# Optimization experiments

Hardware: AMD Instinct MI355X
Metric: run time of the kernel (lower is better)

## Reference

```python
import jax, jax.numpy as jnp
import numpy as np

N_NODES = 50000
N_EDGES = 800000
HIDDEN = 64
DEPTH = 3
NUM_GRAPHS = 256
NUM_CLASSES = 1
BN_EPS = 1e-5


def setup_inputs() -> dict:
    key = jax.random.key(0)
    ks = jax.random.split(key, 12)
    x = jax.random.normal(ks[0], (N_NODES, HIDDEN), dtype=jnp.float32)
    edge_index = jax.random.randint(ks[1], (2, N_EDGES), 0, N_NODES, dtype=jnp.int32)
    batch = jnp.sort(jax.random.randint(ks[2], (N_NODES,), 0, NUM_GRAPHS, dtype=jnp.int32))
    s = 1.0 / np.sqrt(HIDDEN)
    W1 = jax.random.uniform(ks[3], (DEPTH, HIDDEN, HIDDEN), jnp.float32, -s, s)
    b1 = jax.random.uniform(ks[4], (DEPTH, HIDDEN), jnp.float32, -s, s)
    W2 = jax.random.uniform(ks[5], (DEPTH, HIDDEN, HIDDEN), jnp.float32, -s, s)
    b2 = jax.random.uniform(ks[6], (DEPTH, HIDDEN), jnp.float32, -s, s)
    gamma = jnp.ones((DEPTH, HIDDEN), jnp.float32)
    beta = jnp.zeros((DEPTH, HIDDEN), jnp.float32)
    Wf = jax.random.uniform(ks[7], (HIDDEN, NUM_CLASSES), jnp.float32, -s, s)
    bf = jax.random.uniform(ks[8], (NUM_CLASSES,), jnp.float32, -s, s)
    return {"x": x, "edge_index": edge_index, "batch": batch,
            "W1": W1, "b1": b1, "W2": W2, "b2": b2,
            "gamma": gamma, "beta": beta, "Wf": Wf, "bf": bf}


def reference(x, edge_index, batch, W1, b1, W2, b2, gamma, beta, Wf, bf):
    src, dst = edge_index[0], edge_index[1]
    for i in range(DEPTH):
        # GINConv: (1+eps)*x + scatter-add of neighbor features (eps=0)
        agg = jnp.zeros_like(x).at[dst].add(x[src])
        h = x + agg
        h = jax.nn.relu(h @ W1[i] + b1[i])
        h = jax.nn.relu(h @ W2[i] + b2[i])
        # BatchNorm over node dimension (training-mode batch stats)
        mean = h.mean(axis=0)
        var = ((h - mean) ** 2).mean(axis=0)
        h = (h - mean) * jax.lax.rsqrt(var + BN_EPS) * gamma[i] + beta[i]
        x = jax.nn.relu(h)
    pooled = jax.ops.segment_sum(x, batch, num_segments=NUM_GRAPHS)  # [G, H]
    return pooled @ Wf + bf
```

## Files before the change

### kernel.cpp

```cpp
#include <hip/hip_runtime.h>

#define HIDDEN_C 64
#define NCHUNK 256

typedef __attribute__((ext_vector_type(8))) short bf16x8;
typedef __attribute__((ext_vector_type(8))) unsigned short u16x8;
typedef __attribute__((ext_vector_type(4))) float f32x4;

__device__ __forceinline__ float4 f4zero() { return make_float4(0.f, 0.f, 0.f, 0.f); }

__device__ __forceinline__ unsigned short f2bf(float f) {
    unsigned u = __float_as_uint(f);
    u += 0x7FFF + ((u >> 16) & 1);
    return (unsigned short)(u >> 16);
}
__device__ __forceinline__ float bf2f(unsigned short h) {
    return __uint_as_float(((unsigned)h) << 16);
}
__device__ __forceinline__ unsigned short f2h(float f) {
    _Float16 h = (_Float16)f;
    unsigned short u;
    __builtin_memcpy(&u, &h, 2);
    return u;
}
__device__ __forceinline__ float h2f(unsigned short u) {
    _Float16 h;
    __builtin_memcpy(&h, &u, 2);
    return (float)h;
}

__device__ __forceinline__ int swz_idx(int row, int k) {
    return row * 64 + ((((k >> 3) ^ (row & 7)) << 3) | (k & 7));
}

__global__ __launch_bounds__(256) void k_xcvt(const float4* __restrict__ in,
                                              ushort4* __restrict__ out, int n4) {
    int i = blockIdx.x * 256 + threadIdx.x;
    if (i < n4) {
        float4 v = in[i];
        ushort4 o;
        o.x = f2h(v.x); o.y = f2h(v.y); o.z = f2h(v.z); o.w = f2h(v.w);
        out[i] = o;
    }
}

__global__ __launch_bounds__(256) void k_blocksum(const int* __restrict__ deg,
                                                  int* __restrict__ partial, int n) {
    int base = blockIdx.x * 1024 + threadIdx.x * 4;
    int s = 0;
#pragma unroll
    for (int k = 0; k < 4; ++k) {
        int i = base + k;
        if (i < n) s += deg[i];
    }
    __shared__ int red[256];
    red[threadIdx.x] = s;
    __syncthreads();
    for (int d = 128; d > 0; d >>= 1) {
        if (threadIdx.x < d) red[threadIdx.x] += red[threadIdx.x + d];
        __syncthreads();
    }
    if (threadIdx.x == 0) partial[blockIdx.x] = red[0];
}

__global__ __launch_bounds__(256) void k_scanpartial(int* __restrict__ partial,
                                                     int* __restrict__ last_slot,
                                                     int nBlocks, int nE) {
    __shared__ int buf[256];
    int tid = threadIdx.x;
    int v = (tid < nBlocks) ? partial[tid] : 0;
    buf[tid] = v;
    __syncthreads();
    for (int d = 1; d < 256; d <<= 1) {
        int t = (tid >= d) ? buf[tid - d] : 0;
        __syncthreads();
        buf[tid] += t;
        __syncthreads();
    }
    if (tid < nBlocks) partial[tid] = buf[tid] - v;
    if (tid == 0) last_slot[0] = nE;
}

__global__ __launch_bounds__(256) void k_writeptr(const int* __restrict__ deg,
                                                  const int* __restrict__ partial,
                                                  int* __restrict__ outp, int n) {
    int tid = threadIdx.x;
    int base = blockIdx.x * 1024 + tid * 4;
    int d[4];
    int s = 0;
#pragma unroll
    for (int k = 0; k < 4; ++k) {
        int i = base + k;
        d[k] = (i < n) ? deg[i] : 0;
        s += d[k];
    }
    __shared__ int buf[256];
    buf[tid] = s;
    __syncthreads();
    for (int dd = 1; dd < 256; dd <<= 1) {
        int t = (tid >= dd) ? buf[tid - dd] : 0;
        __syncthreads();
        buf[tid] += t;
        __syncthreads();
    }
    int off = partial[blockIdx.x] + buf[tid] - s;
#pragma unroll
    for (int k = 0; k < 4; ++k) {
        int i = base + k;
        if (i < n) {
            outp[i] = off;
            off += d[k];
        }
    }
}

__global__ __launch_bounds__(256) void k_bcount(const int* __restrict__ dst,
                                                int* __restrict__ cnt,
                                                int nE, int chunkSz, int nBuckets) {
    __shared__ int h[1024];
    int c = blockIdx.x, tid = threadIdx.x;
    for (int i = tid; i < nBuckets; i += 256) h[i] = 0;
    __syncthreads();
    int beg = c * chunkSz;
    int end = beg + chunkSz; if (end > nE) end = nE;
    int e = beg + tid;
    for (; e + 256 < end; e += 512) {
        int d0 = dst[e];
        int d1 = dst[e + 256];
        atomicAdd(&h[d0 >> 6], 1);
        atomicAdd(&h[d1 >> 6], 1);
    }
    if (e < end) atomicAdd(&h[dst[e] >> 6], 1);
    __syncthreads();
    for (int i = tid; i < nBuckets; i += 256) cnt[i * NCHUNK + c] = h[i];
}

__global__ __launch_bounds__(256) void k_bscatter(const int* __restrict__ src,
                                                  const int* __restrict__ dst,
                                                  const int* __restrict__ eoff,
                                                  unsigned* __restrict__ ebuf,
                                                  int nE, int chunkSz, int nBuckets) {
    __shared__ int cur[1024];
    int c = blockIdx.x, tid = threadIdx.x;
    for (int i = tid; i < nBuckets; i += 256) cur[i] = eoff[i * NCHUNK + c];
    __syncthreads();
    int beg = c * chunkSz;
    int end = beg + chunkSz; if (end > nE) end = nE;
    int e = beg + tid;
    for (; e + 256 < end; e += 512) {
        int d0 = dst[e];
        int d1 = dst[e + 256];
        int s0 = src[e];
        int s1 = src[e + 256];
        int p0 = atomicAdd(&cur[d0 >> 6], 1);
        int p1 = atomicAdd(&cur[d1 >> 6], 1);
        ebuf[p0] = ((unsigned)(d0 & 63) << 16) | (unsigned)s0;
        ebuf[p1] = ((unsigned)(d1 & 63) << 16) | (unsigned)s1;
    }
    if (e < end) {
        int d = dst[e];
        int pos = atomicAdd(&cur[d >> 6], 1);
        ebuf[pos] = ((unsigned)(d & 63) << 16) | (unsigned)src[e];
    }
}

__global__ __launch_bounds__(256) void k_bfill(const unsigned* __restrict__ ebuf,
                                               const int* __restrict__ eoff,
                                               int* __restrict__ rowptr,
                                               int* __restrict__ col,
                                               int nNodes, int nE, int nBuckets) {
    __shared__ int deg[64], cur[64];
    int b = blockIdx.x, tid = threadIdx.x;
    int lo = eoff[b * NCHUNK];
    int hi = (b + 1 < nBuckets) ? eoff[(b + 1) * NCHUNK] : nE;
    if (tid < 64) deg[tid] = 0;
    __syncthreads();
    for (int e = lo + tid; e < hi; e += 256) atomicAdd(&deg[ebuf[e] >> 16], 1);
    __syncthreads();
    if (tid < 64) {
        int d = deg[tid];
        int s = d;
        for (int o = 1; o < 64; o <<= 1) {
            int t = __shfl_up(s, o, 64);
            if (tid >= o) s += t;
        }
        int st = s - d;
        cur[tid] = lo + st;
        int node = b * 64 + tid;
        if (node < nNodes) rowptr[node] = lo + st;
    }
    __syncthreads();
    for (int e = lo + tid; e < hi; e += 256) {
        unsigned pk = ebuf[e];
        int pos = atomicAdd(&cur[pk >> 16], 1);
        col[pos] = (int)(pk & 0xFFFFu);
    }
}

__global__ __launch_bounds__(256) void k_wprep(const float* __restrict__ W1,
                                               const float* __restrict__ W2,
                                               unsigned short* __restrict__ wt) {
    __shared__ unsigned short s[8192];
    int b = blockIdx.x;
    int layer = b >> 1;
    const float* src = ((b & 1) ? W2 : W1) + (size_t)layer * 4096;
    int tid = threadIdx.x;
    int k = tid >> 2;
    int f0 = (tid & 3) * 16;
    const float* srcp = src + k * 64 + f0;
#pragma unroll
    for (int j4 = 0; j4 < 4; ++j4) {
        float4 wv = *(const float4*)(srcp + j4 * 4);
        float c[4] = {wv.x, wv.y, wv.z, wv.w};
        int f = f0 + j4 * 4;
#pragma unroll
        for (int j = 0; j < 4; ++j) {
            unsigned short h = f2bf(c[j]);
            int ix = swz_idx(f + j, k);
            s[ix] = h;
            s[4096 + ix] = f2bf(c[j] - bf2f(h));
        }
    }
    __syncthreads();
    uint4* dst = (uint4*)(wt + (size_t)b * 8192);
    const uint4* sp = (const uint4*)s;
#pragma unroll
    for (int it = 0; it < 4; ++it) dst[it * 256 + tid] = sp[it * 256 + tid];
}

__global__ __launch_bounds__(256) void k_statred(const float* __restrict__ pstat,
                                                 float* __restrict__ stats, int nb) {
    int j = blockIdx.x;
    int tid = threadIdx.x;
    float s = 0.f;
    for (int b = tid; b < nb; b += 256) s += pstat[(size_t)b * 128 + j];
    __shared__ float red[256];
    red[tid] = s;
    __syncthreads();
    for (int d = 128; d > 0; d >>= 1) {
        if (tid < d) red[tid] += red[tid + d];
        __syncthreads();
    }
    if (tid == 0) stats[j] = red[0];
}

template <bool DOBN>
__global__ __launch_bounds__(256) void k_aggbn(const unsigned short* __restrict__ x16,
                                               const int* __restrict__ rowptr,
                                               const int* __restrict__ col,
                                               const float* __restrict__ stats,
                                               const float* __restrict__ gamma,
                                               const float* __restrict__ beta,
                                               unsigned short* __restrict__ hout,
                                               int nNodes, float invN) {
    int wid = threadIdx.x >> 6;
    int lane = threadIdx.x & 63;
    int g8 = lane >> 3;
    int l8 = lane & 7;
    int n = blockIdx.x * 4 + wid;
    if (n >= nNodes) return;

    float sc[8], sh[8];
    if (DOBN) {
#pragma unroll
        for (int j = 0; j < 8; ++j) {
            int f = l8 * 8 + j;
            float m = stats[f] * invN;
            float var = stats[64 + f] * invN - m * m;
            sc[j] = gamma[f] * rsqrtf(var + 1e-5f);
            sh[j] = beta[f] - m * sc[j];
        }
    }

#define LOADROW8(IDX, OP)                                                    \
    {                                                                        \
        u16x8 uv = *(const u16x8*)(x16 + (size_t)(IDX) * 64 + l8 * 8);       \
        _Pragma("unroll")                                                    \
        for (int j = 0; j < 8; ++j) {                                        \
            float v = h2f(uv[j]);                                            \
            if (DOBN) v = fmaxf(fmaf(v, sc[j], sh[j]), 0.f);                 \
            OP;                                                              \
        }                                                                    \
    }

    float acc[8] = {0.f, 0.f, 0.f, 0.f, 0.f, 0.f, 0.f, 0.f};
    if (g8 == 0) {
        LOADROW8(n, acc[j] = v)
    }

    int lo = rowptr[n], hi = rowptr[n + 1];
    int e = lo;
    for (; e + 16 <= hi; e += 16) {
        int i0 = col[e + g8];
        int i1 = col[e + 8 + g8];
        float t[8];
        LOADROW8(i0, t[j] = v)
        LOADROW8(i1, t[j] += v)
#pragma unroll
        for (int j = 0; j < 8; ++j) acc[j] += t[j];
    }
    for (; e + 8 <= hi; e += 8) {
        int i0 = col[e + g8];
        LOADROW8(i0, acc[j] += v)
    }
    if (e < hi) {
        int ee = e + g8;
        bool ok = ee < hi;
        int idx = col[ok ? ee : (hi - 1)];
        float t[8];
        LOADROW8(idx, t[j] = v)
        if (ok) {
#pragma unroll
            for (int j = 0; j < 8; ++j) acc[j] += t[j];
        }
    }
#undef LOADROW8

#pragma unroll
    for (int j = 0; j < 8; ++j) {
        acc[j] += __shfl_xor(acc[j], 8, 64);
        acc[j] += __shfl_xor(acc[j], 16, 64);
        acc[j] += __shfl_xor(acc[j], 32, 64);
    }

    if (lane < 8) {
        u16x8 o;
#pragma unroll
        for (int j = 0; j < 8; ++j) o[j] = f2h(acc[j]);
        *(u16x8*)(hout + (size_t)n * 64 + lane * 8) = o;
    }
}

__global__ __launch_bounds__(256, 5) void k_mlp(const unsigned short* __restrict__ h_in,
                                                unsigned short* __restrict__ h_out,
                                                const unsigned short* __restrict__ wt1,
                                                const float* __restrict__ b1,
                                                const unsigned short* __restrict__ wt2,
                                                const float* __restrict__ b2,
                                                float* __restrict__ pstat,
                                                int nNodes) {
    __shared__ __align__(16) unsigned short smem16[16384];
    unsigned short* sA_hi = smem16;
    unsigned short* sA_lo = smem16 + 4096;
    unsigned short* sW_hi = smem16 + 8192;
    unsigned short* sW_lo = smem16 + 12288;

    int tid = threadIdx.x;
    int n0 = blockIdx.x * 64;
    int lane = tid & 63;
    int w = tid >> 6;
    int lr = lane & 15;
    int q = lane >> 4;
    int r0 = w * 16;

    uint4 w2r[4];
#pragma unroll
    for (int it = 0; it < 4; ++it) w2r[it] = ((const uint4*)wt2)[it * 256 + tid];

#pragma unroll
    for (int it = 0; it < 2; ++it) {
        int idx = it * 256 + tid;
        int row = idx >> 3, ch = idx & 7;
        u16x8 iv = (u16x8)(0);
        if (n0 + row < nNodes)
            iv = *(const u16x8*)(h_in + (size_t)(n0 + row) * 64 + ch * 8);
        u16x8 hv, lv;
#pragma unroll
        for (int j = 0; j < 8; ++j) {
            float f = h2f(iv[j]);
            unsigned short h = f2bf(f);
            hv[j] = h;
            lv[j] = f2bf(f - bf2f(h));
        }
        int off = row * 64 + ((ch ^ (row & 7)) << 3);
        *(u16x8*)(sA_hi + off) = hv;
        *(u16x8*)(sA_lo + off) = lv;
    }
    {
        uint4* d = (uint4*)sW_hi;
        const uint4* s = (const uint4*)wt1;
#pragma unroll
        for (int it = 0; it < 4; ++it) d[it * 256 + tid] = s[it * 256 + tid];
    }
    __syncthreads();

    f32x4 acc[4];

#define GEMM_SPLIT(BIAS)                                                         \
    {                                                                            \
        int rowA = r0 + lr;                                                      \
        const unsigned short* pah = sA_hi + rowA * 64;                           \
        const unsigned short* pal = sA_lo + rowA * 64;                           \
        int sr = rowA & 7;                                                       \
        bf16x8 ah0 = *(const bf16x8*)(pah + ((q ^ sr) << 3));                    \
        bf16x8 ah1 = *(const bf16x8*)(pah + (((4 + q) ^ sr) << 3));              \
        bf16x8 al0 = *(const bf16x8*)(pal + ((q ^ sr) << 3));                    \
        bf16x8 al1 = *(const bf16x8*)(pal + (((4 + q) ^ sr) << 3));              \
        _Pragma("unroll")                                                        \
        for (int ct = 0; ct < 4; ++ct) {                                         \
            int f = ct * 16 + lr;                                                \
            const unsigned short* pbh = sW_hi + f * 64;                          \
            const unsigned short* pbl = sW_lo + f * 64;                          \
            int sf = f & 7;                                                      \
            bf16x8 bh0 = *(const bf16x8*)(pbh + ((q ^ sf) << 3));                \
            bf16x8 bh1 = *(const bf16x8*)(pbh + (((4 + q) ^ sf) << 3));          \
            bf16x8 bl0 = *(const bf16x8*)(pbl + ((q ^ sf) << 3));                \
            bf16x8 bl1 = *(const bf16x8*)(pbl + (((4 + q) ^ sf) << 3));          \
            float bias = BIAS[f];                                                \
            f32x4 c = {bias, bias, bias, bias};                                  \
            c = __builtin_amdgcn_mfma_f32_16x16x32_bf16(al0, bh0, c, 0, 0, 0);   \
            c = __builtin_amdgcn_mfma_f32_16x16x32_bf16(al1, bh1, c, 0, 0, 0);   \
            c = __builtin_amdgcn_mfma_f32_16x16x32_bf16(ah0, bl0, c, 0, 0, 0);   \
            c = __builtin_amdgcn_mfma_f32_16x16x32_bf16(ah1, bl1, c, 0, 0, 0);   \
            c = __builtin_amdgcn_mfma_f32_16x16x32_bf16(ah0, bh0, c, 0, 0, 0);   \
            c = __builtin_amdgcn_mfma_f32_16x16x32_bf16(ah1, bh1, c, 0, 0, 0);   \
            acc[ct] = c;                                                         \
        }                                                                        \
    }

    GEMM_SPLIT(b1)

    __syncthreads();

#pragma unroll
    for (int ct = 0; ct < 4; ++ct) {
        int f = ct * 16 + lr;
#pragma unroll
        for (int rg = 0; rg < 4; ++rg) {
            int row = r0 + q * 4 + rg;
            float v = fmaxf(acc[ct][rg], 0.f);
            unsigned short h = f2bf(v);
            int ix = swz_idx(row, f);
            sA_hi[ix] = h;
            sA_lo[ix] = f2bf(v - bf2f(h));
        }
    }
    {
        uint4* d = (uint4*)sW_hi;
#pragma unroll
        for (int it = 0; it < 4; ++it) d[it * 256 + tid] = w2r[it];
    }
    __syncthreads();

    GEMM_SPLIT(b2)

    __syncthreads();
#undef GEMM_SPLIT

    float* sS = (float*)sW_hi;
    float* sQ = sS + 256;

#pragma unroll
    for (int ct = 0; ct < 4; ++ct) {
        int f = ct * 16 + lr;
        float sp = 0.f, qp = 0.f;
#pragma unroll
        for (int rg = 0; rg < 4; ++rg) {
            int row = r0 + q * 4 + rg;
            float v = fmaxf(acc[ct][rg], 0.f);
            if (n0 + row < nNodes) {
                unsigned short hv = f2h(v);
                h_out[(size_t)(n0 + row) * 64 + f] = hv;
                float vq = h2f(hv);
                sp += vq;
                qp += vq * vq;
            }
        }
        sp += __shfl_xor(sp, 16, 64); qp += __shfl_xor(qp, 16, 64);
        sp += __shfl_xor(sp, 32, 64); qp += __shfl_xor(qp, 32, 64);
        if (q == 0) {
            sS[w * 64 + f] = sp;
            sQ[w * 64 + f] = qp;
        }
    }
    __syncthreads();
    if (tid < 128) {
        float v;
        if (tid < 64)
            v = sS[tid] + sS[64 + tid] + sS[128 + tid] + sS[192 + tid];
        else {
            int f = tid - 64;
            v = sQ[f] + sQ[64 + f] + sQ[128 + f] + sQ[192 + f];
        }
        pstat[(size_t)blockIdx.x * 128 + tid] = v;
    }
}

__device__ __forceinline__ int lower_bound_dev(const int* a, int n, int key) {
    int lo = 0, hi = n;
    while (lo < hi) {
        int mid = (lo + hi) >> 1;
        if (a[mid] < key) lo = mid + 1; else hi = mid;
    }
    return lo;
}

__global__ __launch_bounds__(256) void k_pool(const unsigned short* __restrict__ x16,
                                              const int* __restrict__ batch,
                                              const float* __restrict__ stats,
                                              const float* __restrict__ gamma,
                                              const float* __restrict__ beta,
                                              const float* __restrict__ Wf,
                                              const float* __restrict__ bf,
                                              float* __restrict__ out,
                                              int nNodes, float invN) {
    int wid = threadIdx.x >> 6;
    int lane = threadIdx.x & 63;
    int grp = lane >> 4;
    int l16 = lane & 15;
    int g = blockIdx.x * 4 + wid;

    float4 sc, sh;
    {
        float4 s  = ((const float4*)stats)[l16];
        float4 q  = ((const float4*)stats)[16 + l16];
        float4 ga = ((const float4*)gamma)[l16];
        float4 be = ((const float4*)beta)[l16];
        float m;
        m = s.x * invN; sc.x = ga.x * rsqrtf(q.x * invN - m * m + 1e-5f); sh.x = be.x - m * sc.x;
        m = s.y * invN; sc.y = ga.y * rsqrtf(q.y * invN - m * m + 1e-5f); sh.y = be.y - m * sc.y;
        m = s.z * invN; sc.z = ga.z * rsqrtf(q.z * invN - m * m + 1e-5f); sh.z = be.z - m * sc.z;
        m = s.w * invN; sc.w = ga.w * rsqrtf(q.w * invN - m * m + 1e-5f); sh.w = be.w - m * sc.w;
    }

    int lo = lower_bound_dev(batch, nNodes, g);
    int hi = lower_bound_dev(batch, nNodes, g + 1);

    float4 acc = f4zero();
    for (int r = lo + grp; r < hi; r += 4) {
        ushort4 uv = *(const ushort4*)(x16 + (size_t)r * 64 + l16 * 4);
        acc.x += fmaxf(fmaf(h2f(uv.x), sc.x, sh.x), 0.f);
        acc.y += fmaxf(fmaf(h2f(uv.y), sc.y, sh.y), 0.f);
        acc.z += fmaxf(fmaf(h2f(uv.z), sc.z, sh.z), 0.f);
        acc.w += fmaxf(fmaf(h2f(uv.w), sc.w, sh.w), 0.f);
    }
    acc.x += __shfl_xor(acc.x, 16, 64); acc.y += __shfl_xor(acc.y, 16, 64);
    acc.z += __shfl_xor(acc.z, 16, 64); acc.w += __shfl_xor(acc.w, 16, 64);
    acc.x += __shfl_xor(acc.x, 32, 64); acc.y += __shfl_xor(acc.y, 32, 64);
    acc.z += __shfl_xor(acc.z, 32, 64); acc.w += __shfl_xor(acc.w, 32, 64);

    float4 wf = ((const float4*)Wf)[l16];
    float p = acc.x * wf.x + acc.y * wf.y + acc.z * wf.z + acc.w * wf.w;
    p += __shfl_xor(p, 1, 64);
    p += __shfl_xor(p, 2, 64);
    p += __shfl_xor(p, 4, 64);
    p += __shfl_xor(p, 8, 64);
    if (lane == 0) out[g] = p + bf[0];
}

extern "C" void kernel_launch(void* const* d_in, const int* in_sizes, int n_in,
                              void* d_out, int out_size, void* d_ws, size_t ws_size,
                              hipStream_t stream) {
    const float* x_in  = (const float*)d_in[0];
    const int*   ei    = (const int*)d_in[1];
    const int*   batch = (const int*)d_in[2];
    const float* W1    = (const float*)d_in[3];
    const float* b1    = (const float*)d_in[4];
    const float* W2    = (const float*)d_in[5];
    const float* b2    = (const float*)d_in[6];
    const float* gamma = (const float*)d_in[7];
    const float* beta  = (const float*)d_in[8];
    const float* Wf    = (const float*)d_in[9];
    const float* bf    = (const float*)d_in[10];

    const int nNodes = in_sizes[0] / HIDDEN_C;
    const int nE = in_sizes[1] / 2;
    const int* src = ei;
    const int* dst = ei + nE;

    const int nBuckets = (nNodes + 63) / 64;
    const int nTot = nBuckets * NCHUNK;
    const int chunkSz = (nE + NCHUNK - 1) / NCHUNK;
    const int scanBlocks = (nTot + 1023) / 1024;
    const float invN = 1.f / (float)nNodes;

    const size_t NH = ((size_t)nNodes * HIDDEN_C * sizeof(unsigned short) + 255) & ~(size_t)255;
    char* ws = (char*)d_ws;
    unsigned short* x16 = (unsigned short*)ws;
    unsigned short* hA  = (unsigned short*)(ws + NH);
    unsigned short* hB  = (unsigned short*)(ws + 2 * NH);
    float*    stats   = (float*)(ws + 3 * NH);
    unsigned short* wtbuf = (unsigned short*)(ws + 3 * NH + 4096);
    float*    pstat   = (float*)(ws + 3 * NH + 4096 + 98304);
    int*      rowptr  = (int*)((char*)pstat + 409600);
    int*      partial = rowptr + nNodes + 64;
    int*      col     = partial + 256;
    unsigned* ebuf    = (unsigned*)hB;
    int*      cnt     = (int*)((char*)hB + (size_t)nE * 4);
    int*      eoff    = cnt + nTot + 64;

    const int mlpGrid = nBuckets;
    const int aggGrid = (nNodes + 3) / 4;
    const int cvtGrid = (nNodes * 16 + 255) / 256;

    k_xcvt<<<cvtGrid, 256, 0, stream>>>((const float4*)x_in, (ushort4*)x16, nNodes * 16);
    k_wprep<<<6, 256, 0, stream>>>(W1, W2, wtbuf);
    k_bcount<<<NCHUNK, 256, 0, stream>>>(dst, cnt, nE, chunkSz, nBuckets);
    k_blocksum<<<scanBlocks, 256, 0, stream>>>(cnt, partial, nTot);
    k_scanpartial<<<1, 256, 0, stream>>>(partial, rowptr + nNodes, scanBlocks, nE);
    k_writeptr<<<scanBlocks, 256, 0, stream>>>(cnt, partial, eoff, nTot);
    k_bscatter<<<NCHUNK, 256, 0, stream>>>(src, dst, eoff, ebuf, nE, chunkSz, nBuckets);
    k_bfill<<<nBuckets, 256, 0, stream>>>(ebuf, eoff, rowptr, col, nNodes, nE, nBuckets);

    const unsigned short* prev_h = x16;
    unsigned short* cur = hA;
    for (int i = 0; i < 3; ++i) {
        if (i == 0) {
            k_aggbn<false><<<aggGrid, 256, 0, stream>>>(prev_h, rowptr, col,
                                                        nullptr, nullptr, nullptr,
                                                        cur, nNodes, invN);
        } else {
            k_aggbn<true><<<aggGrid, 256, 0, stream>>>(prev_h, rowptr, col,
                                                       stats + (size_t)(i - 1) * 128,
                                                       gamma + (size_t)(i - 1) * 64,
                                                       beta + (size_t)(i - 1) * 64,
                                                       cur, nNodes, invN);
        }
        k_mlp<<<mlpGrid, 256, 0, stream>>>(cur, cur,
                                           wtbuf + (size_t)(2 * i) * 8192, b1 + (size_t)i * 64,
                                           wtbuf + (size_t)(2 * i + 1) * 8192, b2 + (size_t)i * 64,
                                           pstat, nNodes);
        k_statred<<<128, 256, 0, stream>>>(pstat, stats + (size_t)i * 128, nBuckets);
        prev_h = cur;
        cur = (cur == hA) ? hB : hA;
    }

    k_pool<<<64, 256, 0, stream>>>(prev_h, batch, stats + 256, gamma + 128, beta + 128,
                                   Wf, bf, (float*)d_out, nNodes, invN);
}
```

Before: 196.4 us.

## Fuse CSR-build preprocessing kernels and replace per-chunk offsets with global atomic bucket cursors

```diff
diff --git a/kernel.cpp b/kernel.cpp
--- a/kernel.cpp
+++ b/kernel.cpp
@@ -33,90 +33,105 @@
     return row * 64 + ((((k >> 3) ^ (row & 7)) << 3) | (k & 7));
 }
 
-__global__ __launch_bounds__(256) void k_xcvt(const float4* __restrict__ in,
-                                              ushort4* __restrict__ out, int n4) {
-    int i = blockIdx.x * 256 + threadIdx.x;
+__global__ __launch_bounds__(256) void k_prep(const float4* __restrict__ xin4,
+                                              ushort4* __restrict__ x16o, int n4,
+                                              const float* __restrict__ W1,
+                                              const float* __restrict__ W2,
+                                              unsigned short* __restrict__ wt,
+                                              const int* __restrict__ dst,
+                                              int* __restrict__ gTot,
+                                              int nE, int chunkSz, int nBuckets) {
+    __shared__ unsigned short s[8192];
+    __shared__ int h[1024];
+    int b = blockIdx.x, tid = threadIdx.x;
+
+    int i = b * 256 + tid;
     if (i < n4) {
-        float4 v = in[i];
+        float4 v = xin4[i];
         ushort4 o;
         o.x = f2h(v.x); o.y = f2h(v.y); o.z = f2h(v.z); o.w = f2h(v.w);
-        out[i] = o;
-    }
-}
-
-__global__ __launch_bounds__(256) void k_blocksum(const int* __restrict__ deg,
-                                                  int* __restrict__ partial, int n) {
-    int base = blockIdx.x * 1024 + threadIdx.x * 4;
-    int s = 0;
-#pragma unroll
-    for (int k = 0; k < 4; ++k) {
-        int i = base + k;
-        if (i < n) s += deg[i];
-    }
-    __shared__ int red[256];
-    red[threadIdx.x] = s;
-    __syncthreads();
-    for (int d = 128; d > 0; d >>= 1) {
-        if (threadIdx.x < d) red[threadIdx.x] += red[threadIdx.x + d];
+        x16o[i] = o;
+    }
+
+    if (b < 6) {
+        int layer = b >> 1;
+        const float* src = ((b & 1) ? W2 : W1) + (size_t)layer * 4096;
+        int k = tid >> 2;
+        int f0 = (tid & 3) * 16;
+        const float* srcp = src + k * 64 + f0;
+#pragma unroll
+        for (int j4 = 0; j4 < 4; ++j4) {
+            float4 wv = *(const float4*)(srcp + j4 * 4);
+            float c[4] = {wv.x, wv.y, wv.z, wv.w};
+            int f = f0 + j4 * 4;
+#pragma unroll
+            for (int j = 0; j < 4; ++j) {
+                unsigned short hh = f2bf(c[j]);
+                int ix = swz_idx(f + j, k);
+                s[ix] = hh;
+                s[4096 + ix] = f2bf(c[j] - bf2f(hh));
+            }
+        }
         __syncthreads();
-    }
-    if (threadIdx.x == 0) partial[blockIdx.x] = red[0];
-}
-
-__global__ __launch_bounds__(256) void k_scanpartial(int* __restrict__ partial,
-                                                     int* __restrict__ last_slot,
-                                                     int nBlocks, int nE) {
-    __shared__ int buf[256];
+        uint4* dstw = (uint4*)(wt + (size_t)b * 8192);
+        const uint4* sp = (const uint4*)s;
+#pragma unroll
+        for (int it = 0; it < 4; ++it) dstw[it * 256 + tid] = sp[it * 256 + tid];
+    }
+
+    if (b < NCHUNK) {
+        for (int j = tid; j < nBuckets; j += 256) h[j] = 0;
+        __syncthreads();
+        int beg = b * chunkSz;
+        int end = beg + chunkSz; if (end > nE) end = nE;
+        int e = beg + tid;
+        for (; e + 256 < end; e += 512) {
+            int d0 = dst[e];
+            int d1 = dst[e + 256];
+            atomicAdd(&h[d0 >> 6], 1);
+            atomicAdd(&h[d1 >> 6], 1);
+        }
+        if (e < end) atomicAdd(&h[dst[e] >> 6], 1);
+        __syncthreads();
+        for (int j = tid; j < nBuckets; j += 256) {
+            int c = h[j];
+            if (c) atomicAdd(&gTot[j], c);
+        }
+    }
+}
+
+__global__ __launch_bounds__(1024) void k_bscan(const int* __restrict__ gTot,
+                                                int* __restrict__ gBase,
+                                                int* __restrict__ gCur,
+                                                int* __restrict__ rowptr,
+                                                int nBuckets, int nNodes, int nE) {
+    __shared__ int buf[1024];
     int tid = threadIdx.x;
-    int v = (tid < nBlocks) ? partial[tid] : 0;
+    int v = (tid < nBuckets) ? gTot[tid] : 0;
     buf[tid] = v;
     __syncthreads();
-    for (int d = 1; d < 256; d <<= 1) {
+    for (int d = 1; d < 1024; d <<= 1) {
         int t = (tid >= d) ? buf[tid - d] : 0;
         __syncthreads();
         buf[tid] += t;
         __syncthreads();
     }
-    if (tid < nBlocks) partial[tid] = buf[tid] - v;
-    if (tid == 0) last_slot[0] = nE;
-}
-
-__global__ __launch_bounds__(256) void k_writeptr(const int* __restrict__ deg,
-                                                  const int* __restrict__ partial,
-                                                  int* __restrict__ outp, int n) {
-    int tid = threadIdx.x;
-    int base = blockIdx.x * 1024 + tid * 4;
-    int d[4];
-    int s = 0;
-#pragma unroll
-    for (int k = 0; k < 4; ++k) {
-        int i = base + k;
-        d[k] = (i < n) ? deg[i] : 0;
-        s += d[k];
-    }
-    __shared__ int buf[256];
-    buf[tid] = s;
-    __syncthreads();
-    for (int dd = 1; dd < 256; dd <<= 1) {
-        int t = (tid >= dd) ? buf[tid - dd] : 0;
-        __syncthreads();
-        buf[tid] += t;
-        __syncthreads();
-    }
-    int off = partial[blockIdx.x] + buf[tid] - s;
-#pragma unroll
-    for (int k = 0; k < 4; ++k) {
-        int i = base + k;
-        if (i < n) {
-            outp[i] = off;
-            off += d[k];
-        }
-    }
-}
-
-__global__ __launch_bounds__(256) void k_bcount(const int* __restrict__ dst,
-                                                int* __restrict__ cnt,
-                                                int nE, int chunkSz, int nBuckets) {
+    if (tid < nBuckets) {
+        int ex = buf[tid] - v;
+        gBase[tid] = ex;
+        gCur[tid] = ex;
+    }
+    if (tid == 0) {
+        gBase[nBuckets] = nE;
+        rowptr[nNodes] = nE;
+    }
+}
+
+__global__ __launch_bounds__(256) void k_bscatter(const int* __restrict__ src,
+                                                  const int* __restrict__ dst,
+                                                  int* __restrict__ gCur,
+                                                  unsigned* __restrict__ ebuf,
+                                                  int nE, int chunkSz, int nBuckets) {
     __shared__ int h[1024];
     int c = blockIdx.x, tid = threadIdx.x;
     for (int i = tid; i < nBuckets; i += 256) h[i] = 0;
@@ -125,54 +140,43 @@
     int end = beg + chunkSz; if (end > nE) end = nE;
     int e = beg + tid;
     for (; e + 256 < end; e += 512) {
-        int d0 = dst[e];
-        int d1 = dst[e + 256];
-        atomicAdd(&h[d0 >> 6], 1);
-        atomicAdd(&h[d1 >> 6], 1);
+        atomicAdd(&h[dst[e] >> 6], 1);
+        atomicAdd(&h[dst[e + 256] >> 6], 1);
     }
     if (e < end) atomicAdd(&h[dst[e] >> 6], 1);
     __syncthreads();
-    for (int i = tid; i < nBuckets; i += 256) cnt[i * NCHUNK + c] = h[i];
-}
-
-__global__ __launch_bounds__(256) void k_bscatter(const int* __restrict__ src,
-                                                  const int* __restrict__ dst,
-                                                  const int* __restrict__ eoff,
-                                                  unsigned* __restrict__ ebuf,
-                                                  int nE, int chunkSz, int nBuckets) {
-    __shared__ int cur[1024];
-    int c = blockIdx.x, tid = threadIdx.x;
-    for (int i = tid; i < nBuckets; i += 256) cur[i] = eoff[i * NCHUNK + c];
-    __syncthreads();
-    int beg = c * chunkSz;
-    int end = beg + chunkSz; if (end > nE) end = nE;
-    int e = beg + tid;
+    for (int i = tid; i < nBuckets; i += 256) {
+        int cc = h[i];
+        h[i] = cc ? atomicAdd(&gCur[i], cc) : 0;
+    }
+    __syncthreads();
+    e = beg + tid;
     for (; e + 256 < end; e += 512) {
         int d0 = dst[e];
         int d1 = dst[e + 256];
         int s0 = src[e];
         int s1 = src[e + 256];
-        int p0 = atomicAdd(&cur[d0 >> 6], 1);
-        int p1 = atomicAdd(&cur[d1 >> 6], 1);
+        int p0 = atomicAdd(&h[d0 >> 6], 1);
+        int p1 = atomicAdd(&h[d1 >> 6], 1);
         ebuf[p0] = ((unsigned)(d0 & 63) << 16) | (unsigned)s0;
         ebuf[p1] = ((unsigned)(d1 & 63) << 16) | (unsigned)s1;
     }
     if (e < end) {
         int d = dst[e];
-        int pos = atomicAdd(&cur[d >> 6], 1);
+        int pos = atomicAdd(&h[d >> 6], 1);
         ebuf[pos] = ((unsigned)(d & 63) << 16) | (unsigned)src[e];
     }
 }
 
 __global__ __launch_bounds__(256) void k_bfill(const unsigned* __restrict__ ebuf,
-                                               const int* __restrict__ eoff,
+                                               const int* __restrict__ gBase,
                                                int* __restrict__ rowptr,
                                                int* __restrict__ col,
-                                               int nNodes, int nE, int nBuckets) {
+                                               int nNodes, int nBuckets) {
     __shared__ int deg[64], cur[64];
     int b = blockIdx.x, tid = threadIdx.x;
-    int lo = eoff[b * NCHUNK];
-    int hi = (b + 1 < nBuckets) ? eoff[(b + 1) * NCHUNK] : nE;
+    int lo = gBase[b];
+    int hi = gBase[b + 1];
     if (tid < 64) deg[tid] = 0;
     __syncthreads();
     for (int e = lo + tid; e < hi; e += 256) atomicAdd(&deg[ebuf[e] >> 16], 1);
@@ -195,37 +199,6 @@
         int pos = atomicAdd(&cur[pk >> 16], 1);
         col[pos] = (int)(pk & 0xFFFFu);
     }
-}
-
-__global__ __launch_bounds__(256) void k_wprep(const float* __restrict__ W1,
-                                               const float* __restrict__ W2,
-                                               unsigned short* __restrict__ wt) {
-    __shared__ unsigned short s[8192];
-    int b = blockIdx.x;
-    int layer = b >> 1;
-    const float* src = ((b & 1) ? W2 : W1) + (size_t)layer * 4096;
-    int tid = threadIdx.x;
-    int k = tid >> 2;
-    int f0 = (tid & 3) * 16;
-    const float* srcp = src + k * 64 + f0;
-#pragma unroll
-    for (int j4 = 0; j4 < 4; ++j4) {
-        float4 wv = *(const float4*)(srcp + j4 * 4);
-        float c[4] = {wv.x, wv.y, wv.z, wv.w};
-        int f = f0 + j4 * 4;
-#pragma unroll
-        for (int j = 0; j < 4; ++j) {
-            unsigned short h = f2bf(c[j]);
-            int ix = swz_idx(f + j, k);
-            s[ix] = h;
-            s[4096 + ix] = f2bf(c[j] - bf2f(h));
-        }
-    }
-    __syncthreads();
-    uint4* dst = (uint4*)(wt + (size_t)b * 8192);
-    const uint4* sp = (const uint4*)s;
-#pragma unroll
-    for (int it = 0; it < 4; ++it) dst[it * 256 + tid] = sp[it * 256 + tid];
 }
 
 __global__ __launch_bounds__(256) void k_statred(const float* __restrict__ pstat,
@@ -569,9 +542,7 @@
     const int* dst = ei + nE;
 
     const int nBuckets = (nNodes + 63) / 64;
-    const int nTot = nBuckets * NCHUNK;
     const int chunkSz = (nE + NCHUNK - 1) / NCHUNK;
-    const int scanBlocks = (nTot + 1023) / 1024;
     const float invN = 1.f / (float)nNodes;
 
     const size_t NH = ((size_t)nNodes * HIDDEN_C * sizeof(unsigned short) + 255) & ~(size_t)255;
@@ -583,24 +554,22 @@
     unsigned short* wtbuf = (unsigned short*)(ws + 3 * NH + 4096);
     float*    pstat   = (float*)(ws + 3 * NH + 4096 + 98304);
     int*      rowptr  = (int*)((char*)pstat + 409600);
-    int*      partial = rowptr + nNodes + 64;
-    int*      col     = partial + 256;
+    int*      gTot    = rowptr + nNodes + 64;
+    int*      gBase   = gTot + nBuckets + 16;
+    int*      gCur    = gBase + nBuckets + 16;
+    int*      col     = gCur + nBuckets + 16;
     unsigned* ebuf    = (unsigned*)hB;
-    int*      cnt     = (int*)((char*)hB + (size_t)nE * 4);
-    int*      eoff    = cnt + nTot + 64;
 
     const int mlpGrid = nBuckets;
     const int aggGrid = (nNodes + 3) / 4;
     const int cvtGrid = (nNodes * 16 + 255) / 256;
 
-    k_xcvt<<<cvtGrid, 256, 0, stream>>>((const float4*)x_in, (ushort4*)x16, nNodes * 16);
-    k_wprep<<<6, 256, 0, stream>>>(W1, W2, wtbuf);
-    k_bcount<<<NCHUNK, 256, 0, stream>>>(dst, cnt, nE, chunkSz, nBuckets);
-    k_blocksum<<<scanBlocks, 256, 0, stream>>>(cnt, partial, nTot);
-    k_scanpartial<<<1, 256, 0, stream>>>(partial, rowptr + nNodes, scanBlocks, nE);
-    k_writeptr<<<scanBlocks, 256, 0, stream>>>(cnt, partial, eoff, nTot);
-    k_bscatter<<<NCHUNK, 256, 0, stream>>>(src, dst, eoff, ebuf, nE, chunkSz, nBuckets);
-    k_bfill<<<nBuckets, 256, 0, stream>>>(ebuf, eoff, rowptr, col, nNodes, nE, nBuckets);
+    hipMemsetAsync(gTot, 0, (size_t)nBuckets * sizeof(int), stream);
+    k_prep<<<cvtGrid, 256, 0, stream>>>((const float4*)x_in, (ushort4*)x16, nNodes * 16,
+                                        W1, W2, wtbuf, dst, gTot, nE, chunkSz, nBuckets);
+    k_bscan<<<1, 1024, 0, stream>>>(gTot, gBase, gCur, rowptr, nBuckets, nNodes, nE);
+    k_bscatter<<<NCHUNK, 256, 0, stream>>>(src, dst, gCur, ebuf, nE, chunkSz, nBuckets);
+    k_bfill<<<nBuckets, 256, 0, stream>>>(ebuf, gBase, rowptr, col, nNodes, nBuckets);
 
     const unsigned short* prev_h = x16;
     unsigned short* cur = hA;
```

After: 202.9 us. 3.3% more time.
